# Optimization experiments

Hardware: AMD Instinct MI355X
Metric: run time of the kernel (lower is better)

## Reference

```python
import jax, jax.numpy as jnp
import numpy as np
from jax import lax

# FlowNet-C correlation hyperparameters (match init_kwargs)
PAD = 20          # pad_size
K = 1             # kernel_size
MAXD = 20         # max_displacement
S1 = 1            # stride1 (output stride)
S2 = 2            # stride2 (displacement stride)


def setup_inputs() -> dict:
    key = jax.random.key(0)
    k1, k2 = jax.random.split(key)
    B, C, H, W = 8, 256, 64, 96
    input1 = jax.random.normal(k1, (B, C, H, W), dtype=jnp.float32)
    input2 = jax.random.normal(k2, (B, C, H, W), dtype=jnp.float32)
    return {"input1": input1, "input2": input2}


def reference(input1, input2):
    B, C, H, W = input1.shape
    kr = (K - 1) // 2                    # kernel radius (0 for K=1)
    border = MAXD + kr                   # border in padded coords
    pH, pW = H + 2 * PAD, W + 2 * PAD
    out_h = (pH - 2 * border) // S1      # = H for PAD == MAXD, S1 == 1
    out_w = (pW - 2 * border) // S1
    R = MAXD // S2                       # displacement grid radius = 10
    D = 2 * R + 1                        # grid width = 21 -> 441 channels
    sumelems = jnp.float32(K * K * C)

    p1 = jnp.pad(input1, ((0, 0), (0, 0), (PAD, PAD), (PAD, PAD)))
    p2 = jnp.pad(input2, ((0, 0), (0, 0), (PAD, PAD), (PAD, PAD)))

    # centered patch of input1 (kernel_size == 1, stride1 == 1)
    f1 = lax.dynamic_slice(p1, (0, 0, border, border), (B, C, out_h, out_w))

    # displacement offsets, row-major over (dy, dx) as in correlation_cuda
    disps = jnp.stack(
        jnp.meshgrid(jnp.arange(D), jnp.arange(D), indexing="ij"), axis=-1
    ).reshape(-1, 2)  # [D*D, 2]

    def corr_one(d):
        y0 = border + (d[0] - R) * S2
        x0 = border + (d[1] - R) * S2
        f2 = lax.dynamic_slice(p2, (0, 0, y0, x0), (B, C, out_h, out_w))
        # dot product over channels, normalized by kernel_size^2 * C
        return jnp.sum(f1 * f2, axis=1) / sumelems  # [B, out_h, out_w]

    out = lax.map(corr_one, disps)               # [D*D, B, out_h, out_w]
    return jnp.transpose(out, (1, 0, 2, 3))      # [B, D*D, out_h, out_w]
```

## Files before the change

### kernel.cpp

```cpp
#include <hip/hip_runtime.h>
#include <cstdint>
#include <cstddef>


typedef short bf16x8 __attribute__((ext_vector_type(8)));
typedef float f32x4  __attribute__((ext_vector_type(4)));

constexpr int B_ = 8, C_ = 256, H_ = 64, W_ = 96, D_ = 21;
constexpr int THREADS = 512;
constexpr int CSTR = H_ * W_;
constexpr size_t IMG = (size_t)C_ * CSTR;
constexpr int PLANE = 1536;
constexpr int LSZ = D_ * 49;

__global__ __launch_bounds__(THREADS, 4) void corr_mfma(
    const float* __restrict__ in1,
    const float* __restrict__ in2,
    float* __restrict__ out)
{
    __shared__ uint4 ldsq[2 * PLANE];
    __shared__ float lout[2 * LSZ];

    const int id  = blockIdx.x;
    const int b   = id & 7;
    const int p   = (id >> 3) & 1;
    const int y   = id >> 4;
    const int tid = threadIdx.x;
    const int lane = tid & 63, li = lane & 15, gl = lane >> 4, wid = tid >> 6;

    const int mw = (wid < 2) ? 0 : (wid < 5) ? 16 : 32;
    const int vw = (wid == 0 || wid == 2) ? 0 : (wid == 4 || wid == 6) ? 32 : 16;

    const int dylo = (y >= 21) ? 0 : ((21 - y) >> 1);
    const int dyhi = min(20, (83 - y) >> 1);

    auto cvt = [&](const float (&f)[8], int gdst) {
        uint hv[4], lv[4];
        #pragma unroll
        for (int q = 0; q < 4; ++q) {
            uint a0 = __float_as_uint(f[2*q]), a1 = __float_as_uint(f[2*q+1]);
            hv[q] = (a1 & 0xFFFF0000u) | (a0 >> 16);
            float r0 = f[2*q]   - __uint_as_float(a0 & 0xFFFF0000u);
            float r1 = f[2*q+1] - __uint_as_float(a1 & 0xFFFF0000u);
            lv[q] = (__float_as_uint(r1) & 0xFFFF0000u) | (__float_as_uint(r0) >> 16);
        }
        ldsq[gdst]         = uint4{hv[0], hv[1], hv[2], hv[3]};
        ldsq[gdst + PLANE] = uint4{lv[0], lv[1], lv[2], lv[3]};
    };

    auto stage_now = [&](const float* src) {
        #pragma unroll
        for (int n = 0; n < 3; ++n) {
            int t = tid + n * THREADS;
            int v = t % 48, cg = t / 48;
            const float* g = src + (size_t)cg * 8 * CSTR + 2 * v;
            float f[8];
            #pragma unroll
            for (int j = 0; j < 8; ++j) f[j] = g[(size_t)j * CSTR];
            cvt(f, v * 32 + (cg ^ (v & 7)));
        }
    };

    stage_now(in1 + (size_t)b * IMG + (size_t)y * W_ + p);
    for (int z = tid; z < 2 * LSZ; z += THREADS) lout[z] = 0.f;
    __syncthreads();

    bf16x8 ah[8], al[8];
    {
        const int rA = mw + li;
        #pragma unroll
        for (int k0 = 0; k0 < 8; ++k0) {
            int off = rA * 32 + ((4 * k0 + gl) ^ (rA & 7));
            ah[k0] = *(const bf16x8*)&ldsq[off];
            al[k0] = *(const bf16x8*)&ldsq[PLANE + off];
        }
    }
    __syncthreads();

    stage_now(in2 + (size_t)b * IMG + (size_t)(y + 2 * dylo - 20) * W_ + p);

    int offB[8];
    {
        const int rB = vw + li;
        #pragma unroll
        for (int k0 = 0; k0 < 8; ++k0)
            offB[k0] = rB * 32 + ((4 * k0 + gl) ^ (rB & 7));
    }
    int pg[3], gof[3];
    {
        #pragma unroll
        for (int n = 0; n < 3; ++n) {
            int t = tid + n * THREADS;
            int v = t % 48, cg = t / 48;
            gof[n] = cg * 8 * CSTR + 2 * v;
            pg[n]  = v * 32 + (cg ^ (v & 7));
        }
    }
    const float* gb2 = in2 + (size_t)b * IMG + p;
    __syncthreads();

    float pf0[8], pf1[8], pf2[8];
    for (int dy = dylo; dy <= dyhi; ++dy) {
        const bool pref = dy < dyhi;
        if (pref) {
            const int ro = (y + 2 * (dy + 1) - 20) * W_;
            #pragma unroll
            for (int j = 0; j < 8; ++j) pf0[j] = gb2[gof[0] + ro + j * CSTR];
            #pragma unroll
            for (int j = 0; j < 8; ++j) pf1[j] = gb2[gof[1] + ro + j * CSTR];
            #pragma unroll
            for (int j = 0; j < 8; ++j) pf2[j] = gb2[gof[2] + ro + j * CSTR];
        }

        if (wid < 7) {
            f32x4 aH = {0.f,0.f,0.f,0.f}, aL = {0.f,0.f,0.f,0.f},
                  aM = {0.f,0.f,0.f,0.f};
            #define KSTEP(k0) {                                                  \
                bf16x8 bh = *(const bf16x8*)&ldsq[offB[k0]];                     \
                bf16x8 bl = *(const bf16x8*)&ldsq[PLANE + offB[k0]];             \
                aL = __builtin_amdgcn_mfma_f32_16x16x32_bf16(al[k0], bh, aL, 0,0,0); \
                aM = __builtin_amdgcn_mfma_f32_16x16x32_bf16(ah[k0], bl, aM, 0,0,0); \
                aH = __builtin_amdgcn_mfma_f32_16x16x32_bf16(ah[k0], bh, aH, 0,0,0); }
            KSTEP(0) KSTEP(1) KSTEP(2) KSTEP(3)
            KSTEP(4) KSTEP(5) KSTEP(6) KSTEP(7)
            #undef KSTEP

            const int lb = dy & 1;
            #pragma unroll
            for (int rr = 0; rr < 4; ++rr) {
                int u = mw + gl * 4 + rr, v = vw + li, dx = v - u + 10;
                if ((unsigned)dx < 21u)
                    lout[lb * LSZ + dx * 49 + u] =
                        (aH[rr] + (aL[rr] + aM[rr])) * (1.f / 256.f);
            }
        }
        __syncthreads();

        if (pref) {
            cvt(pf0, pg[0]); cvt(pf1, pg[1]); cvt(pf2, pg[2]);
        }
        if (wid < 7 && lane < 48) {
            const int lb = dy & 1;
            #pragma unroll
            for (int q = 0; q < 3; ++q) {
                int dx = wid + 7 * q;
                float val = lout[lb * LSZ + dx * 49 + lane];
                out[(((size_t)(b * 441 + dy * D_ + dx)) * H_ + y) * W_
                    + p + 2 * lane] = val;
                lout[lb * LSZ + dx * 49 + lane] = 0.f;
            }
        }
        __syncthreads();
    }

    for (int dy = 0; dy < D_; ++dy) {
        if (dy >= dylo && dy <= dyhi) continue;
        for (int z = tid; z < D_ * 48; z += THREADS) {
            int dx = z / 48, u = z - dx * 48;
            out[(((size_t)(b * 441 + dy * D_ + dx)) * H_ + y) * W_
                + p + 2 * u] = 0.f;
        }
    }
}

extern "C" void kernel_launch(void* const* d_in, const int* in_sizes, int n_in,
                              void* d_out, int out_size, void* d_ws, size_t ws_size,
                              hipStream_t stream) {
    const float* in1 = (const float*)d_in[0];
    const float* in2 = (const float*)d_in[1];
    float* out = (float*)d_out;
    (void)in_sizes; (void)n_in; (void)d_ws; (void)ws_size; (void)out_size;
    dim3 grid(B_ * H_ * 2);
    corr_mfma<<<grid, dim3(THREADS), 0, stream>>>(in1, in2, out);
}
```

Before: 336.6 us.

## Precompute bf16 hi/lo split in workspace pass, stream row tiles into LDS

Adds a prepass kernel that converts both inputs once into packed bf16 hi/lo row tiles in the workspace, laid out contiguously per (input, batch, parity, row). The correlation kernel then copies these tiles straight into double-buffered LDS with coalesced 16-byte loads, instead of doing strided fp32 gathers and repeating the split conversion for every displacement row. This costs an extra kernel launch and a full workspace write and read. It also uses twice the LDS per block, with launch bounds lowered to 2 blocks per CU. The old kernel is kept as a fallback for when no workspace of the needed size is given.

```diff
diff --git a/kernel.cpp b/kernel.cpp
--- a/kernel.cpp
+++ b/kernel.cpp
@@ -7,19 +7,61 @@
 typedef float f32x4  __attribute__((ext_vector_type(4)));
 
 constexpr int B_ = 8, C_ = 256, H_ = 64, W_ = 96, D_ = 21;
-constexpr int THREADS = 512;
 constexpr int CSTR = H_ * W_;
 constexpr size_t IMG = (size_t)C_ * CSTR;
-constexpr int PLANE = 1536;
-constexpr int LSZ = D_ * 49;
-
-__global__ __launch_bounds__(THREADS, 4) void corr_mfma(
-    const float* __restrict__ in1,
-    const float* __restrict__ in2,
-    float* __restrict__ out)
+constexpr int RT = 3072;
+constexpr size_t WS_NEED = (size_t)2 * 8 * 2 * 64 * RT * 16;
+
+__device__ __forceinline__ size_t rtbase(int inp, int b, int p, int y) {
+    return ((size_t)(((inp * 8 + b) * 2 + p) * 64 + y)) * RT;
+}
+
+__device__ __forceinline__ void packhl(const float (&f)[8], uint4& hi, uint4& lo) {
+    uint hv[4], lv[4];
+    #pragma unroll
+    for (int q = 0; q < 4; ++q) {
+        uint a0 = __float_as_uint(f[2*q]), a1 = __float_as_uint(f[2*q+1]);
+        hv[q] = (a1 & 0xFFFF0000u) | (a0 >> 16);
+        float r0 = f[2*q]   - __uint_as_float(a0 & 0xFFFF0000u);
+        float r1 = f[2*q+1] - __uint_as_float(a1 & 0xFFFF0000u);
+        lv[q] = (__float_as_uint(r1) & 0xFFFF0000u) | (__float_as_uint(r0) >> 16);
+    }
+    hi = uint4{hv[0], hv[1], hv[2], hv[3]};
+    lo = uint4{lv[0], lv[1], lv[2], lv[3]};
+}
+
+__global__ __launch_bounds__(512, 2) void cvt_split(
+    const float* __restrict__ in1, const float* __restrict__ in2,
+    uint4* __restrict__ cv)
 {
-    __shared__ uint4 ldsq[2 * PLANE];
-    __shared__ float lout[2 * LSZ];
+    const int id  = blockIdx.x;
+    const int inp = id >> 9;
+    const int rem = id & 511;
+    const int b = rem >> 6, y = rem & 63;
+    const int tid = threadIdx.x;
+    const float* src = (inp ? in2 : in1) + (size_t)b * IMG + (size_t)y * W_;
+
+    #pragma unroll
+    for (int r = 0; r < 6; ++r) {
+        int t  = tid + r * 512;
+        int cg = t / 96, x = t - cg * 96;
+        int p  = x & 1,  v = x >> 1;
+        float f[8];
+        #pragma unroll
+        for (int j = 0; j < 8; ++j) f[j] = src[(size_t)(cg * 8 + j) * CSTR + x];
+        uint4 hi, lo;
+        packhl(f, hi, lo);
+        size_t g = rtbase(inp, b, p, y) + cg * 48 + v;
+        cv[g]        = hi;
+        cv[g + 1536] = lo;
+    }
+}
+
+__global__ __launch_bounds__(512, 2) void corr_mfma2(
+    const uint4* __restrict__ cv, float* __restrict__ out)
+{
+    __shared__ uint4 lds[2 * RT];
+    __shared__ float lout[D_ * 49];
 
     const int id  = blockIdx.x;
     const int b   = id & 7;
@@ -34,24 +76,140 @@
     const int dylo = (y >= 21) ? 0 : ((21 - y) >> 1);
     const int dyhi = min(20, (83 - y) >> 1);
 
+    {
+        const uint4* s = cv + rtbase(0, b, p, y);
+        #pragma unroll
+        for (int n = 0; n < 6; ++n) {
+            int g = (n * 8 + wid) * 64 + lane;
+            lds[g] = s[g];
+        }
+    }
+    for (int z = tid; z < D_ * 49; z += 512) lout[z] = 0.f;
+    __syncthreads();
+
+    bf16x8 ah[8], al[8];
+    int offB[8];
+    {
+        const int rA = mw + li, rB = vw + li;
+        #pragma unroll
+        for (int k0 = 0; k0 < 8; ++k0) {
+            int oa = (4 * k0 + gl) * 48 + rA;
+            ah[k0] = *(const bf16x8*)&lds[oa];
+            al[k0] = *(const bf16x8*)&lds[oa + 1536];
+            offB[k0] = (4 * k0 + gl) * 48 + rB;
+        }
+    }
+    __syncthreads();
+
+    {
+        const uint4* s = cv + rtbase(1, b, p, y + 2 * dylo - 20);
+        #pragma unroll
+        for (int n = 0; n < 6; ++n) {
+            int g = (n * 8 + wid) * 64 + lane;
+            lds[g] = s[g];
+        }
+    }
+    __syncthreads();
+
+    int cur = 0;
+    uint4 st[6];
+    for (int dy = dylo; dy <= dyhi; ++dy) {
+        const bool more = dy < dyhi;
+        if (more) {
+            const uint4* s = cv + rtbase(1, b, p, y + 2 * (dy + 1) - 20);
+            #pragma unroll
+            for (int n = 0; n < 6; ++n) st[n] = s[(n * 8 + wid) * 64 + lane];
+        }
+
+        if (wid < 7) {
+            const int cb = cur * RT;
+            f32x4 aH = {0.f,0.f,0.f,0.f}, aL = {0.f,0.f,0.f,0.f},
+                  aM = {0.f,0.f,0.f,0.f};
+            #define KSTEP(k0) {                                                  \
+                bf16x8 bh = *(const bf16x8*)&lds[cb + offB[k0]];                 \
+                bf16x8 bl = *(const bf16x8*)&lds[cb + 1536 + offB[k0]];          \
+                aL = __builtin_amdgcn_mfma_f32_16x16x32_bf16(al[k0], bh, aL, 0,0,0); \
+                aM = __builtin_amdgcn_mfma_f32_16x16x32_bf16(ah[k0], bl, aM, 0,0,0); \
+                aH = __builtin_amdgcn_mfma_f32_16x16x32_bf16(ah[k0], bh, aH, 0,0,0); }
+            KSTEP(0) KSTEP(1) KSTEP(2) KSTEP(3)
+            KSTEP(4) KSTEP(5) KSTEP(6) KSTEP(7)
+            #undef KSTEP
+            #pragma unroll
+            for (int rr = 0; rr < 4; ++rr) {
+                int u = mw + gl * 4 + rr, v = vw + li, dx = v - u + 10;
+                if ((unsigned)dx < 21u)
+                    lout[dx * 49 + u] = (aH[rr] + (aL[rr] + aM[rr])) * (1.f / 256.f);
+            }
+        }
+        __syncthreads();
+
+        if (more) {
+            const int nb = (cur ^ 1) * RT;
+            #pragma unroll
+            for (int n = 0; n < 6; ++n) lds[nb + (n * 8 + wid) * 64 + lane] = st[n];
+        }
+        float ov[3];
+        const bool do_out = (wid < 7) && (lane < 48);
+        if (do_out) {
+            #pragma unroll
+            for (int q = 0; q < 3; ++q) {
+                int dx = wid + 7 * q;
+                ov[q] = lout[dx * 49 + lane];
+                lout[dx * 49 + lane] = 0.f;
+            }
+        }
+        __syncthreads();
+        if (do_out) {
+            #pragma unroll
+            for (int q = 0; q < 3; ++q) {
+                int dx = wid + 7 * q;
+                out[(((size_t)(b * 441 + dy * D_ + dx)) * H_ + y) * W_
+                    + p + 2 * lane] = ov[q];
+            }
+        }
+        cur ^= 1;
+    }
+
+    for (int dy = 0; dy < D_; ++dy) {
+        if (dy >= dylo && dy <= dyhi) continue;
+        for (int z = tid; z < D_ * 48; z += 512) {
+            int dx = z / 48, u = z - dx * 48;
+            out[(((size_t)(b * 441 + dy * D_ + dx)) * H_ + y) * W_
+                + p + 2 * u] = 0.f;
+        }
+    }
+}
+
+constexpr int PLANE = 1536;
+constexpr int LSZ = D_ * 49;
+
+__global__ __launch_bounds__(512, 4) void corr_fb(
+    const float* __restrict__ in1, const float* __restrict__ in2,
+    float* __restrict__ out)
+{
+    __shared__ uint4 ldsq[2 * PLANE];
+    __shared__ float lout[2 * LSZ];
+    const int id  = blockIdx.x;
+    const int b   = id & 7;
+    const int p   = (id >> 3) & 1;
+    const int y   = id >> 4;
+    const int tid = threadIdx.x;
+    const int lane = tid & 63, li = lane & 15, gl = lane >> 4, wid = tid >> 6;
+    const int mw = (wid < 2) ? 0 : (wid < 5) ? 16 : 32;
+    const int vw = (wid == 0 || wid == 2) ? 0 : (wid == 4 || wid == 6) ? 32 : 16;
+    const int dylo = (y >= 21) ? 0 : ((21 - y) >> 1);
+    const int dyhi = min(20, (83 - y) >> 1);
+
     auto cvt = [&](const float (&f)[8], int gdst) {
-        uint hv[4], lv[4];
-        #pragma unroll
-        for (int q = 0; q < 4; ++q) {
-            uint a0 = __float_as_uint(f[2*q]), a1 = __float_as_uint(f[2*q+1]);
-            hv[q] = (a1 & 0xFFFF0000u) | (a0 >> 16);
-            float r0 = f[2*q]   - __uint_as_float(a0 & 0xFFFF0000u);
-            float r1 = f[2*q+1] - __uint_as_float(a1 & 0xFFFF0000u);
-            lv[q] = (__float_as_uint(r1) & 0xFFFF0000u) | (__float_as_uint(r0) >> 16);
-        }
-        ldsq[gdst]         = uint4{hv[0], hv[1], hv[2], hv[3]};
-        ldsq[gdst + PLANE] = uint4{lv[0], lv[1], lv[2], lv[3]};
+        uint4 hi, lo;
+        packhl(f, hi, lo);
+        ldsq[gdst]         = hi;
+        ldsq[gdst + PLANE] = lo;
     };
-
     auto stage_now = [&](const float* src) {
         #pragma unroll
         for (int n = 0; n < 3; ++n) {
-            int t = tid + n * THREADS;
+            int t = tid + n * 512;
             int v = t % 48, cg = t / 48;
             const float* g = src + (size_t)cg * 8 * CSTR + 2 * v;
             float f[8];
@@ -62,9 +220,8 @@
     };
 
     stage_now(in1 + (size_t)b * IMG + (size_t)y * W_ + p);
-    for (int z = tid; z < 2 * LSZ; z += THREADS) lout[z] = 0.f;
-    __syncthreads();
-
+    for (int z = tid; z < 2 * LSZ; z += 512) lout[z] = 0.f;
+    __syncthreads();
     bf16x8 ah[8], al[8];
     {
         const int rA = mw + li;
@@ -76,9 +233,7 @@
         }
     }
     __syncthreads();
-
     stage_now(in2 + (size_t)b * IMG + (size_t)(y + 2 * dylo - 20) * W_ + p);
-
     int offB[8];
     {
         const int rB = vw + li;
@@ -90,7 +245,7 @@
     {
         #pragma unroll
         for (int n = 0; n < 3; ++n) {
-            int t = tid + n * THREADS;
+            int t = tid + n * 512;
             int v = t % 48, cg = t / 48;
             gof[n] = cg * 8 * CSTR + 2 * v;
             pg[n]  = v * 32 + (cg ^ (v & 7));
@@ -111,7 +266,6 @@
             #pragma unroll
             for (int j = 0; j < 8; ++j) pf2[j] = gb2[gof[2] + ro + j * CSTR];
         }
-
         if (wid < 7) {
             f32x4 aH = {0.f,0.f,0.f,0.f}, aL = {0.f,0.f,0.f,0.f},
                   aM = {0.f,0.f,0.f,0.f};
@@ -124,7 +278,6 @@
             KSTEP(0) KSTEP(1) KSTEP(2) KSTEP(3)
             KSTEP(4) KSTEP(5) KSTEP(6) KSTEP(7)
             #undef KSTEP
-
             const int lb = dy & 1;
             #pragma unroll
             for (int rr = 0; rr < 4; ++rr) {
@@ -135,10 +288,7 @@
             }
         }
         __syncthreads();
-
-        if (pref) {
-            cvt(pf0, pg[0]); cvt(pf1, pg[1]); cvt(pf2, pg[2]);
-        }
+        if (pref) { cvt(pf0, pg[0]); cvt(pf1, pg[1]); cvt(pf2, pg[2]); }
         if (wid < 7 && lane < 48) {
             const int lb = dy & 1;
             #pragma unroll
@@ -152,10 +302,9 @@
         }
         __syncthreads();
     }
-
     for (int dy = 0; dy < D_; ++dy) {
         if (dy >= dylo && dy <= dyhi) continue;
-        for (int z = tid; z < D_ * 48; z += THREADS) {
+        for (int z = tid; z < D_ * 48; z += 512) {
             int dx = z / 48, u = z - dx * 48;
             out[(((size_t)(b * 441 + dy * D_ + dx)) * H_ + y) * W_
                 + p + 2 * u] = 0.f;
@@ -169,7 +318,12 @@
     const float* in1 = (const float*)d_in[0];
     const float* in2 = (const float*)d_in[1];
     float* out = (float*)d_out;
-    (void)in_sizes; (void)n_in; (void)d_ws; (void)ws_size; (void)out_size;
-    dim3 grid(B_ * H_ * 2);
-    corr_mfma<<<grid, dim3(THREADS), 0, stream>>>(in1, in2, out);
-}
+    (void)in_sizes; (void)n_in; (void)out_size;
+    if (d_ws != nullptr && ws_size >= WS_NEED) {
+        uint4* cv = (uint4*)d_ws;
+        cvt_split<<<dim3(1024), dim3(512), 0, stream>>>(in1, in2, cv);
+        corr_mfma2<<<dim3(1024), dim3(512), 0, stream>>>(cv, out);
+    } else {
+        corr_fb<<<dim3(1024), dim3(512), 0, stream>>>(in1, in2, out);
+    }
+}
```

After: 324.5 us. 3.6% less time.
